# Kernel tuning notes

Measured on AMD Instinct MI355X. Metric: run time of the kernel, lower is better.

The kernel has to match this reference:

```python
import jax, jax.numpy as jnp
import numpy as np

N_NODES = 200000
N_EDGES = 800000
NODE_IN = 133
EDGE_IN = 14
HID = 128
DEPTH = 4
NUM_GRAPHS = 4096


def _linear_init(key, fan_in, fan_out):
    # torch nn.Linear default init: U(-1/sqrt(fan_in), 1/sqrt(fan_in))
    kw, kb = jax.random.split(key)
    bound = 1.0 / np.sqrt(fan_in)
    W = jax.random.uniform(kw, (fan_in, fan_out), jnp.float32, -bound, bound)
    b = jax.random.uniform(kb, (fan_out,), jnp.float32, -bound, bound)
    return W, b


def setup_inputs() -> dict:
    key = jax.random.key(0)
    ks = jax.random.split(key, 8)
    x = jax.random.normal(ks[0], (N_NODES, NODE_IN), jnp.float32)
    edge_index = jax.random.randint(ks[1], (2, N_EDGES), 0, N_NODES, jnp.int64)
    revedge_index = jax.random.randint(ks[2], (N_EDGES,), 0, N_EDGES, jnp.int64)
    edge_attr = jax.random.normal(ks[3], (N_EDGES, EDGE_IN), jnp.float32)
    batch = jnp.sort(jax.random.randint(ks[4], (N_NODES,), 0, NUM_GRAPHS, jnp.int64))
    W1, b1 = _linear_init(ks[5], NODE_IN + EDGE_IN, HID)
    W2, b2 = _linear_init(ks[6], HID, HID)
    W3, b3 = _linear_init(ks[7], NODE_IN + HID, HID)
    return {"x": x, "edge_attr": edge_attr, "W1": W1, "b1": b1, "W2": W2,
            "b2": b2, "W3": W3, "b3": b3, "edge_index": edge_index,
            "revedge_index": revedge_index, "batch": batch,
            "num_graphs": NUM_GRAPHS}


def reference(x, edge_attr, W1, b1, W2, b2, W3, b3,
              edge_index, revedge_index, batch, num_graphs):
    num_nodes = x.shape[0]
    src, dst = edge_index[0], edge_index[1]
    # initial directed edge messages: [E, node_in + edge_in] -> [E, HID]
    init_msg = jnp.concatenate([x[src], edge_attr], axis=1)
    h0 = jax.nn.relu(init_msg @ W1 + b1)
    h = h0
    for _ in range(DEPTH - 1):
        # sum incoming messages at each node, gather back to edges, remove reverse edge
        node_sum = jax.ops.segment_sum(h, dst, num_segments=num_nodes)
        m = node_sum[src] - h[revedge_index]
        h = jax.nn.relu(h0 + m @ W2 + b2)
    # aggregate final edge messages at destination nodes
    v_msg = jax.ops.segment_sum(h, dst, num_segments=num_nodes)
    z = jnp.concatenate([x, v_msg], axis=1)
    node_attr = jax.nn.relu(z @ W3 + b3)  # dropout is identity in eval mode
    # global mean pool over graphs
    sums = jax.ops.segment_sum(node_attr, batch, num_segments=num_graphs)
    counts = jax.ops.segment_sum(jnp.ones((num_nodes,), node_attr.dtype), batch,
                                 num_segments=num_graphs)
    return sums / jnp.maximum(counts, 1.0)[:, None]
```

## Files before the change

kernel.cpp:

```cpp
#include <hip/hip_runtime.h>

#define N_NODES 200000
#define N_EDGES 800000
#define NODE_IN 133
#define EDGE_IN 14
#define HID 128
#define NUM_GRAPHS 4096

#define SCAN_CHUNK 2048
#define SCAN_NBLK ((N_NODES + SCAN_CHUNK - 1) / SCAN_CHUNK)

#define MT 64
#define MT2 128

#define K1_PAD 160
#define K1_STRIDE 168
#define K2_PAD 128
#define K2_STRIDE 136
#define K3_PAD 288
#define K3_STRIDE 296
#define KE_PAD 32
#define KE_STRIDE 40

typedef unsigned short u16;
typedef unsigned char u8;
typedef short bf16x8 __attribute__((ext_vector_type(8)));
typedef float f32x4 __attribute__((ext_vector_type(4)));

__device__ __forceinline__ float bu2f(unsigned s) {
    return __uint_as_float(s << 16);
}
__device__ __forceinline__ u16 f2bu(float f) {
    unsigned u = __float_as_uint(f);
    return (u16)((u + 0x7FFFu + ((u >> 16) & 1u)) >> 16);
}
__device__ __forceinline__ u16 f2bt(float f) {
    return (u16)(__float_as_uint(f) >> 16);
}
__device__ __forceinline__ float e42f(unsigned b) {
    unsigned E = (b >> 4) & 0xF, M = b & 7u;
    if (E == 0) return (float)M * 0.001953125f;
    return __uint_as_float(((E - 7u + 127u) << 23) | (M << 20));
}
__device__ __forceinline__ u8 f2e4(float f) {
    if (!(f > 0.f)) return 0;
    if (f >= 448.f) return 0x7E;
    unsigned u = __float_as_uint(f);
    int e = (int)((u >> 23) & 0xFF) - 127;
    if (e < -6) {
        int q = (int)rintf(f * 512.f);
        return (u8)q;
    }
    unsigned m = u & 0x7FFFFF;
    unsigned keep = m >> 20, rem = m & 0xFFFFF;
    keep += (rem > 0x80000u || (rem == 0x80000u && (keep & 1u))) ? 1u : 0u;
    unsigned E = (unsigned)(e + 7);
    if (keep == 8u) { keep = 0u; E++; }
    return (u8)((E << 4) | keep);
}

#if defined(__has_builtin)
#if __has_builtin(__builtin_amdgcn_cvt_f32_fp8) && __has_builtin(__builtin_amdgcn_cvt_pk_fp8_f32)
#define HW_FP8 1
#endif
#endif

#if defined(HW_FP8)
#define FP8_DEC(dw, s) __builtin_amdgcn_cvt_f32_fp8((int)(dw), (s))
__device__ __forceinline__ unsigned fp8_pk(float a, float b) {
    a = fminf(fmaxf(a, 0.f), 448.f);
    b = fminf(fmaxf(b, 0.f), 448.f);
    return (unsigned)__builtin_amdgcn_cvt_pk_fp8_f32(a, b, 0, false) & 0xFFFFu;
}
#else
#define FP8_DEC(dw, s) e42f(((dw) >> (8 * (s))) & 0xFFu)
__device__ __forceinline__ unsigned fp8_pk(float a, float b) {
    return (unsigned)f2e4(a) | ((unsigned)f2e4(b) << 8);
}
#endif

__device__ __forceinline__ int clampi(int v, int hi) {
    return v < 0 ? 0 : (v >= hi ? hi - 1 : v);
}

__device__ __forceinline__ void acc16(float* a, const uint4 v) {
    a[0]  += FP8_DEC(v.x, 0); a[1]  += FP8_DEC(v.x, 1);
    a[2]  += FP8_DEC(v.x, 2); a[3]  += FP8_DEC(v.x, 3);
    a[4]  += FP8_DEC(v.y, 0); a[5]  += FP8_DEC(v.y, 1);
    a[6]  += FP8_DEC(v.y, 2); a[7]  += FP8_DEC(v.y, 3);
    a[8]  += FP8_DEC(v.z, 0); a[9]  += FP8_DEC(v.z, 1);
    a[10] += FP8_DEC(v.z, 2); a[11] += FP8_DEC(v.z, 3);
    a[12] += FP8_DEC(v.w, 0); a[13] += FP8_DEC(v.w, 1);
    a[14] += FP8_DEC(v.w, 2); a[15] += FP8_DEC(v.w, 3);
}

__global__ __launch_bounds__(256) void k_prep3(const float* __restrict__ W1,
                                               const float* __restrict__ W2,
                                               const float* __restrict__ W3,
                                               u16* __restrict__ WT1,
                                               u16* __restrict__ WT2,
                                               u16* __restrict__ WT3) {
    int idx = blockIdx.x * 256 + threadIdx.x;
    const int n1 = HID * K1_STRIDE, n2 = HID * K2_STRIDE, n3 = HID * K3_STRIDE;
    if (idx < n1) {
        const int n = idx / K1_STRIDE, k = idx % K1_STRIDE;
        WT1[idx] = (k < NODE_IN + EDGE_IN) ? f2bu(W1[k * HID + n]) : (u16)0;
    } else if ((idx -= n1) < n2) {
        const int n = idx / K2_STRIDE, k = idx % K2_STRIDE;
        WT2[idx] = (k < HID) ? f2bu(W2[k * HID + n]) : (u16)0;
    } else if ((idx -= n2) < n3) {
        const int n = idx / K3_STRIDE, k = idx % K3_STRIDE;
        WT3[idx] = (k < NODE_IN + HID) ? f2bu(W3[k * HID + n]) : (u16)0;
    }
}

__global__ __launch_bounds__(256) void k_hist(const int* __restrict__ dst,
                                              int* __restrict__ cnt) {
    const int e = blockIdx.x * 256 + threadIdx.x;
    if (e < N_EDGES) atomicAdd(&cnt[clampi(dst[e], N_NODES)], 1);
}

__global__ __launch_bounds__(256) void k_scan1(const int* __restrict__ cnt,
                                               int* __restrict__ local,
                                               int* __restrict__ partial) {
    __shared__ int tsum[256];
    const int b = blockIdx.x, t = threadIdx.x;
    const int base = b * SCAN_CHUNK + t * 8;
    int v[8];
    int s = 0;
#pragma unroll
    for (int i = 0; i < 8; i++) {
        const int idx = base + i;
        v[i] = (idx < N_NODES) ? cnt[idx] : 0;
        s += v[i];
    }
    tsum[t] = s;
    __syncthreads();
    for (int ofs = 1; ofs < 256; ofs <<= 1) {
        const int add = (t >= ofs) ? tsum[t - ofs] : 0;
        __syncthreads();
        tsum[t] += add;
        __syncthreads();
    }
    int excl = (t == 0) ? 0 : tsum[t - 1];
    if (t == 255) partial[b] = tsum[255];
#pragma unroll
    for (int i = 0; i < 8; i++) {
        const int idx = base + i;
        if (idx < N_NODES) local[idx] = excl;
        excl += v[i];
    }
}

__global__ __launch_bounds__(256) void k_scan2(int* __restrict__ partial) {
    __shared__ int s[256];
    const int t = threadIdx.x;
    s[t] = (t < SCAN_NBLK) ? partial[t] : 0;
    __syncthreads();
    for (int ofs = 1; ofs < 256; ofs <<= 1) {
        const int add = (t >= ofs) ? s[t - ofs] : 0;
        __syncthreads();
        s[t] += add;
        __syncthreads();
    }
    if (t < SCAN_NBLK) partial[t] = (t == 0) ? 0 : s[t - 1];
}

__global__ __launch_bounds__(256) void k_scan3(const int* __restrict__ local,
                                               const int* __restrict__ partial,
                                               int* __restrict__ row_ptr,
                                               int* __restrict__ cursor) {
    const int idx = blockIdx.x * 256 + threadIdx.x;
    if (idx <= N_NODES) {
        const int v = (idx == N_NODES) ? N_EDGES
                                       : local[idx] + partial[idx / SCAN_CHUNK];
        row_ptr[idx] = v;
        if (idx < N_NODES) cursor[idx] = v;
    }
}

__global__ __launch_bounds__(256) void k_place(const int* __restrict__ dst,
                                               int* __restrict__ cursor,
                                               int* __restrict__ eidx,
                                               int* __restrict__ inv) {
    const int e = blockIdx.x * 256 + threadIdx.x;
    if (e < N_EDGES) {
        const int slot = atomicAdd(&cursor[clampi(dst[e], N_NODES)], 1);
        eidx[slot] = e;
        inv[e] = slot;
    }
}

__global__ __launch_bounds__(256) void k_setup(const int* __restrict__ eidx,
                                               const int* __restrict__ src,
                                               const int* __restrict__ rev,
                                               const int* __restrict__ inv,
                                               const float* __restrict__ ea,
                                               int* __restrict__ src_d,
                                               int* __restrict__ rev_d,
                                               u16* __restrict__ ea_d) {
    const int j = blockIdx.x * 256 + threadIdx.x;
    if (j >= N_EDGES) return;
    const int e = clampi(eidx[j], N_EDGES);
    src_d[j] = src[e];
    rev_d[j] = inv[clampi(rev[e], N_EDGES)];
    const float2* er = (const float2*)(ea + (size_t)e * EDGE_IN);
    u16 v[16];
#pragma unroll
    for (int k = 0; k < 7; k++) {
        const float2 u = er[k];
        v[2 * k] = f2bu(u.x);
        v[2 * k + 1] = f2bu(u.y);
    }
    v[14] = 0; v[15] = 0;
    uint4 o1, o2;
    o1.x = (unsigned)v[0] | ((unsigned)v[1] << 16);
    o1.y = (unsigned)v[2] | ((unsigned)v[3] << 16);
    o1.z = (unsigned)v[4] | ((unsigned)v[5] << 16);
    o1.w = (unsigned)v[6] | ((unsigned)v[7] << 16);
    o2.x = (unsigned)v[8] | ((unsigned)v[9] << 16);
    o2.y = (unsigned)v[10] | ((unsigned)v[11] << 16);
    o2.z = (unsigned)v[12] | ((unsigned)v[13] << 16);
    o2.w = 0;
    uint4* dstp = (uint4*)(ea_d + (size_t)j * 16);
    dstp[0] = o1;
    dstp[1] = o2;
}

__global__ __launch_bounds__(256) void k_gather(const u8* __restrict__ h,
                                                const int* __restrict__ row_ptr,
                                                u8* __restrict__ node_sum) {
    const long long idx = (long long)blockIdx.x * 256 + threadIdx.x;
    const int n = (int)(idx >> 3);
    if (n >= N_NODES) return;
    const int c16 = (int)(idx & 7) << 4;
    const int beg = row_ptr[n], end = row_ptr[n + 1];
    float a[16];
#pragma unroll
    for (int i = 0; i < 16; i++) a[i] = 0.f;
    int j = beg;
    for (; j + 4 <= end; j += 4) {
        const uint4 v0 = *(const uint4*)(h + (long long)j * HID + c16);
        const uint4 v1 = *(const uint4*)(h + (long long)(j + 1) * HID + c16);
        const uint4 v2 = *(const uint4*)(h + (long long)(j + 2) * HID + c16);
        const uint4 v3 = *(const uint4*)(h + (long long)(j + 3) * HID + c16);
        acc16(a, v0); acc16(a, v1); acc16(a, v2); acc16(a, v3);
    }
    for (; j < end; j++) {
        const uint4 v = *(const uint4*)(h + (long long)j * HID + c16);
        acc16(a, v);
    }
    uint4 o;
    o.x = fp8_pk(a[0], a[1])   | (fp8_pk(a[2], a[3])   << 16);
    o.y = fp8_pk(a[4], a[5])   | (fp8_pk(a[6], a[7])   << 16);
    o.z = fp8_pk(a[8], a[9])   | (fp8_pk(a[10], a[11]) << 16);
    o.w = fp8_pk(a[12], a[13]) | (fp8_pk(a[14], a[15]) << 16);
    *(uint4*)(node_sum + (long long)n * HID + c16) = o;
}


__global__ __launch_bounds__(256) void k_xw(const float* __restrict__ x,
                                            const u16* __restrict__ WT1,
                                            u16* __restrict__ xw) {
    __shared__ u16 A[MT * K1_STRIDE];
    const int n0 = blockIdx.x * MT;
    const int t = threadIdx.x;
    const int lane = t & 63, wv = t >> 6;
    for (int rr = 0; rr < 16; rr++) {
        const int row = wv * 16 + rr;
        const int n = n0 + row;
        const float* xr = x + (size_t)n * NODE_IN;
        u16* dstr = &A[row * K1_STRIDE];
        dstr[lane] = f2bu(xr[lane]);
        dstr[64 + lane] = f2bu(xr[64 + lane]);
        if (lane < 5) dstr[128 + lane] = f2bu(xr[128 + lane]);
        if (lane < K1_PAD - NODE_IN) dstr[NODE_IN + lane] = 0;
    }
    __syncthreads();

    const int wm = wv & 1, wn = wv >> 1;
    const int lr = lane & 15, lk = (lane >> 4) * 8;
    f32x4 acc[2][4];
#pragma unroll
    for (int m = 0; m < 2; m++)
#pragma unroll
        for (int n = 0; n < 4; n++) acc[m][n] = (f32x4){0.f, 0.f, 0.f, 0.f};

    const int ar0 = (wm * 32 + lr) * K1_STRIDE + lk;
#pragma unroll
    for (int ks = 0; ks < K1_PAD / 32; ks++) {
        const int kk = ks * 32;
        const bf16x8 a0 = *(const bf16x8*)&A[ar0 + kk];
        const bf16x8 a1 = *(const bf16x8*)&A[ar0 + 16 * K1_STRIDE + kk];
#pragma unroll
        for (int n = 0; n < 4; n++) {
            const bf16x8 b = *(const bf16x8*)&WT1[(size_t)(wn * 64 + n * 16 + lr) * K1_STRIDE + kk + lk];
            acc[0][n] = __builtin_amdgcn_mfma_f32_16x16x32_bf16(a0, b, acc[0][n], 0, 0, 0);
            acc[1][n] = __builtin_amdgcn_mfma_f32_16x16x32_bf16(a1, b, acc[1][n], 0, 0, 0);
        }
    }

    const int lr4 = lane >> 4;
#pragma unroll
    for (int n = 0; n < 4; n++) {
        const int col = wn * 64 + n * 16 + lr;
#pragma unroll
        for (int m = 0; m < 2; m++)
#pragma unroll
            for (int j = 0; j < 4; j++) {
                const int nd = n0 + wm * 32 + m * 16 + lr4 * 4 + j;
                xw[(size_t)nd * HID + col] = f2bu(acc[m][n][j]);
            }
    }
}

__global__ __launch_bounds__(256) void k_init3(const u16* __restrict__ xw,
                                               const u16* __restrict__ ea_d,
                                               const u16* __restrict__ WT1,
                                               const float* __restrict__ b1,
                                               const int* __restrict__ src_d,
                                               u8* __restrict__ h0) {
    __shared__ u16 Aea[MT * KE_STRIDE];
    __shared__ u16 W1e[HID * KE_PAD];
    __shared__ u16 Sacc[MT * K2_STRIDE];
    __shared__ float b1s[HID];
    const int e0 = blockIdx.x * MT;
    const int t = threadIdx.x;

    const int prow = t >> 2, pj = t & 3;
    const int ps = clampi(src_d[e0 + prow], N_NODES);
    uint4 xv[4];
#pragma unroll
    for (int q = 0; q < 4; q++)
        xv[q] = *(const uint4*)(xw + (size_t)ps * HID + pj * 32 + q * 8);

    for (int i = t; i < HID * KE_PAD; i += 256) {
        const int n = i >> 5, k = i & 31;
        W1e[i] = (k < EDGE_IN) ? WT1[n * K1_STRIDE + NODE_IN + k] : (u16)0;
    }
    if (t < HID) b1s[t] = b1[t];
    {
        const int row = t >> 2, q = t & 3;
        const uint2 v = *(const uint2*)(ea_d + (size_t)(e0 + row) * 16 + q * 4);
        *(uint2*)&Aea[row * KE_STRIDE + q * 4] = v;
        uint2 z; z.x = 0; z.y = 0;
        *(uint2*)&Aea[row * KE_STRIDE + 16 + q * 4] = z;
    }
    __syncthreads();

    const int lane = t & 63, wid = t >> 6;
    const int wm = wid & 1, wn = wid >> 1;
    const int lr = lane & 15, lk = (lane >> 4) * 8;
    f32x4 acc[2][4];
#pragma unroll
    for (int m = 0; m < 2; m++)
#pragma unroll
        for (int n = 0; n < 4; n++) acc[m][n] = (f32x4){0.f, 0.f, 0.f, 0.f};

    {
        const bf16x8 a0 = *(const bf16x8*)&Aea[(wm * 32 + lr) * KE_STRIDE + lk];
        const bf16x8 a1 = *(const bf16x8*)&Aea[(wm * 32 + 16 + lr) * KE_STRIDE + lk];
#pragma unroll
        for (int n = 0; n < 4; n++) {
            const bf16x8 b = *(const bf16x8*)&W1e[(wn * 64 + n * 16 + lr) * KE_PAD + lk];
            acc[0][n] = __builtin_amdgcn_mfma_f32_16x16x32_bf16(a0, b, acc[0][n], 0, 0, 0);
            acc[1][n] = __builtin_amdgcn_mfma_f32_16x16x32_bf16(a1, b, acc[1][n], 0, 0, 0);
        }
    }

    const int lr4 = lane >> 4;
#pragma unroll
    for (int n = 0; n < 4; n++) {
        const int col = wn * 64 + n * 16 + lr;
#pragma unroll
        for (int m = 0; m < 2; m++)
#pragma unroll
            for (int j = 0; j < 4; j++) {
                const int row = wm * 32 + m * 16 + lr4 * 4 + j;
                Sacc[row * K2_STRIDE + col] = f2bu(acc[m][n][j]);
            }
    }
    __syncthreads();

    const long long e = e0 + prow;
#pragma unroll
    for (int q = 0; q < 4; q++) {
        const int c8 = pj * 32 + q * 8;
        const uint4 sv = *(const uint4*)&Sacc[prow * K2_STRIDE + c8];
        const float4 ba = *(const float4*)&b1s[c8];
        const float4 bbv = *(const float4*)&b1s[c8 + 4];
        const float v0 = bu2f(sv.x & 0xFFFFu) + bu2f(xv[q].x & 0xFFFFu) + ba.x;
        const float v1 = bu2f(sv.x >> 16)     + bu2f(xv[q].x >> 16)     + ba.y;
        const float v2 = bu2f(sv.y & 0xFFFFu) + bu2f(xv[q].y & 0xFFFFu) + ba.z;
        const float v3 = bu2f(sv.y >> 16)     + bu2f(xv[q].y >> 16)     + ba.w;
        const float v4 = bu2f(sv.z & 0xFFFFu) + bu2f(xv[q].z & 0xFFFFu) + bbv.x;
        const float v5 = bu2f(sv.z >> 16)     + bu2f(xv[q].z >> 16)     + bbv.y;
        const float v6 = bu2f(sv.w & 0xFFFFu) + bu2f(xv[q].w & 0xFFFFu) + bbv.z;
        const float v7 = bu2f(sv.w >> 16)     + bu2f(xv[q].w >> 16)     + bbv.w;
        uint2 o;
        o.x = fp8_pk(v0, v1) | (fp8_pk(v2, v3) << 16);
        o.y = fp8_pk(v4, v5) | (fp8_pk(v6, v7) << 16);
        *(uint2*)(h0 + e * HID + c8) = o;
    }
}

__global__ __launch_bounds__(512) void k_msg_mfma(const u8* __restrict__ ns,
                                                  const u8* __restrict__ h,
                                                  const u8* __restrict__ h0g,
                                                  const u16* __restrict__ WT2,
                                                  const float* __restrict__ b2,
                                                  const int* __restrict__ src_d,
                                                  const int* __restrict__ rev_d,
                                                  u8* __restrict__ hn) {
    __shared__ u16 A[MT2 * K2_STRIDE];
    __shared__ float b2s[HID];
    const int e0 = blockIdx.x * MT2;
    const int t = threadIdx.x;

    const int prow = t >> 2, pj = t & 3;
    const long long pe = e0 + prow;
    uint2 h0v[4];
#pragma unroll
    for (int q = 0; q < 4; q++)
        h0v[q] = *(const uint2*)(h0g + pe * HID + pj * 32 + q * 8);

    if (t < HID) b2s[t] = b2[t];
    {
        const int s = clampi(src_d[e0 + prow], N_NODES);
        const int r = clampi(rev_d[e0 + prow], N_EDGES);
        const u8* nsr = ns + (size_t)s * HID + pj * 32;
        const u8* hr = h + (size_t)r * HID + pj * 32;
        u16* dstr = &A[prow * K2_STRIDE + pj * 32];
#pragma unroll
        for (int q = 0; q < 4; q++) {
            const uint2 nv = *(const uint2*)(nsr + q * 8);
            const uint2 hv = *(const uint2*)(hr + q * 8);
            union { bf16x8 v; u16 s[8]; } o;
            o.s[0] = f2bt(FP8_DEC(nv.x, 0) - FP8_DEC(hv.x, 0));
            o.s[1] = f2bt(FP8_DEC(nv.x, 1) - FP8_DEC(hv.x, 1));
            o.s[2] = f2bt(FP8_DEC(nv.x, 2) - FP8_DEC(hv.x, 2));
            o.s[3] = f2bt(FP8_DEC(nv.x, 3) - FP8_DEC(hv.x, 3));
            o.s[4] = f2bt(FP8_DEC(nv.y, 0) - FP8_DEC(hv.y, 0));
            o.s[5] = f2bt(FP8_DEC(nv.y, 1) - FP8_DEC(hv.y, 1));
            o.s[6] = f2bt(FP8_DEC(nv.y, 2) - FP8_DEC(hv.y, 2));
            o.s[7] = f2bt(FP8_DEC(nv.y, 3) - FP8_DEC(hv.y, 3));
            *(bf16x8*)(dstr + q * 8) = o.v;
        }
    }
    __syncthreads();

    const int lane = t & 63, wid = t >> 6;
    const int wm = wid & 3, wn = wid >> 2;
    const int lr = lane & 15, lk = (lane >> 4) * 8;
    f32x4 acc[2][4];
#pragma unroll
    for (int m = 0; m < 2; m++)
#pragma unroll
        for (int n = 0; n < 4; n++) acc[m][n] = (f32x4){0.f, 0.f, 0.f, 0.f};

    const int ar0 = (wm * 32 + lr) * K2_STRIDE + lk;
#pragma unroll
    for (int ks = 0; ks < K2_PAD / 32; ks++) {
        const int kk = ks * 32;
        const bf16x8 a0 = *(const bf16x8*)&A[ar0 + kk];
        const bf16x8 a1 = *(const bf16x8*)&A[ar0 + 16 * K2_STRIDE + kk];
#pragma unroll
        for (int n = 0; n < 4; n++) {
            const bf16x8 b = *(const bf16x8*)&WT2[(size_t)(wn * 64 + n * 16 + lr) * K2_STRIDE + kk + lk];
            acc[0][n] = __builtin_amdgcn_mfma_f32_16x16x32_bf16(a0, b, acc[0][n], 0, 0, 0);
            acc[1][n] = __builtin_amdgcn_mfma_f32_16x16x32_bf16(a1, b, acc[1][n], 0, 0, 0);
        }
    }

    __syncthreads();
    const int lr4 = lane >> 4;
#pragma unroll
    for (int n = 0; n < 4; n++) {
        const int col = wn * 64 + n * 16 + lr;
#pragma unroll
        for (int m = 0; m < 2; m++)
#pragma unroll
            for (int j = 0; j < 4; j++) {
                const int row = wm * 32 + m * 16 + lr4 * 4 + j;
                A[row * K2_STRIDE + col] = f2bt(acc[m][n][j]);
            }
    }
    __syncthreads();

#pragma unroll
    for (int q = 0; q < 4; q++) {
        const int c8 = pj * 32 + q * 8;
        const uint4 sv = *(const uint4*)&A[prow * K2_STRIDE + c8];
        const float4 ba = *(const float4*)&b2s[c8];
        const float4 bbv = *(const float4*)&b2s[c8 + 4];
        const float v0 = bu2f(sv.x & 0xFFFFu) + FP8_DEC(h0v[q].x, 0) + ba.x;
        const float v1 = bu2f(sv.x >> 16)     + FP8_DEC(h0v[q].x, 1) + ba.y;
        const float v2 = bu2f(sv.y & 0xFFFFu) + FP8_DEC(h0v[q].x, 2) + ba.z;
        const float v3 = bu2f(sv.y >> 16)     + FP8_DEC(h0v[q].x, 3) + ba.w;
        const float v4 = bu2f(sv.z & 0xFFFFu) + FP8_DEC(h0v[q].y, 0) + bbv.x;
        const float v5 = bu2f(sv.z >> 16)     + FP8_DEC(h0v[q].y, 1) + bbv.y;
        const float v6 = bu2f(sv.w & 0xFFFFu) + FP8_DEC(h0v[q].y, 2) + bbv.z;
        const float v7 = bu2f(sv.w >> 16)     + FP8_DEC(h0v[q].y, 3) + bbv.w;
        uint2 o;
        o.x = fp8_pk(v0, v1) | (fp8_pk(v2, v3) << 16);
        o.y = fp8_pk(v4, v5) | (fp8_pk(v6, v7) << 16);
        *(uint2*)(hn + pe * HID + c8) = o;
    }
}

__global__ __launch_bounds__(512) void k_node_mfma(const float* __restrict__ x,
                                                   const u8* __restrict__ h,
                                                   const int* __restrict__ row_ptr,
                                                   const u16* __restrict__ WT3,
                                                   const float* __restrict__ b3,
                                                   u16* __restrict__ node_attr) {
    __shared__ u16 A[MT * K3_STRIDE];
    const int n0 = blockIdx.x * MT;
    const int t = threadIdx.x;
    const int lane = t & 63, wv = t >> 6;
    const int wm = wv & 1, wn = wv >> 1;
    const int lr = lane & 15, lk = (lane >> 4) * 8;

    {
        const int vrow = wv * 8 + (lane >> 3);
        const int vn = n0 + vrow;
        const int c16 = (lane & 7) << 4;
        const int beg = row_ptr[vn], end = row_ptr[vn + 1];
        float a[16];
#pragma unroll
        for (int i = 0; i < 16; i++) a[i] = 0.f;
        int j = beg;
        for (; j + 4 <= end; j += 4) {
            const uint4 v0 = *(const uint4*)(h + (long long)j * HID + c16);
            const uint4 v1 = *(const uint4*)(h + (long long)(j + 1) * HID + c16);
            const uint4 v2 = *(const uint4*)(h + (long long)(j + 2) * HID + c16);
            const uint4 v3 = *(const uint4*)(h + (long long)(j + 3) * HID + c16);
            acc16(a, v0); acc16(a, v1); acc16(a, v2); acc16(a, v3);
        }
        for (; j < end; j++) {
            const uint4 v = *(const uint4*)(h + (long long)j * HID + c16);
            acc16(a, v);
        }
        u16* vd = &A[vrow * K3_STRIDE + NODE_IN + c16];
#pragma unroll
        for (int i = 0; i < 16; i++) vd[i] = f2bt(a[i]);
    }

    for (int rr = 0; rr < 8; rr++) {
        const int row = wv * 8 + rr;
        const int n = n0 + row;
        const float* xr = x + (size_t)n * NODE_IN;
        u16* dstr = &A[row * K3_STRIDE];
        dstr[lane] = f2bu(xr[lane]);
        dstr[64 + lane] = f2bu(xr[64 + lane]);
        if (lane < 5) dstr[128 + lane] = f2bu(xr[128 + lane]);
        if (lane < K3_PAD - (NODE_IN + HID))
            dstr[NODE_IN + HID + lane] = 0;
    }
    __syncthreads();

    f32x4 acc[2][2];
#pragma unroll
    for (int m = 0; m < 2; m++)
#pragma unroll
        for (int n = 0; n < 2; n++) acc[m][n] = (f32x4){0.f, 0.f, 0.f, 0.f};
    const int ar0 = (wm * 32 + lr) * K3_STRIDE + lk;

    for (int ks = 0; ks < K3_PAD / 32; ks++) {
        const int kk = ks * 32;
        const bf16x8 a0 = *(const bf16x8*)&A[ar0 + kk];
        const bf16x8 a1 = *(const bf16x8*)&A[ar0 + 16 * K3_STRIDE + kk];
#pragma unroll
        for (int n = 0; n < 2; n++) {
            const bf16x8 b = *(const bf16x8*)&WT3[(size_t)(wn * 32 + n * 16 + lr) * K3_STRIDE + kk + lk];
            acc[0][n] = __builtin_amdgcn_mfma_f32_16x16x32_bf16(a0, b, acc[0][n], 0, 0, 0);
            acc[1][n] = __builtin_amdgcn_mfma_f32_16x16x32_bf16(a1, b, acc[1][n], 0, 0, 0);
        }
    }

    const int lr4 = lane >> 4;
#pragma unroll
    for (int n = 0; n < 2; n++) {
        const int col = wn * 32 + n * 16 + lr;
        const float bias = b3[col];
#pragma unroll
        for (int m = 0; m < 2; m++)
#pragma unroll
            for (int j = 0; j < 4; j++) {
                const int nd = n0 + wm * 32 + m * 16 + lr4 * 4 + j;
                float v = acc[m][n][j] + bias;
                node_attr[(size_t)nd * HID + col] = f2bu(v > 0.f ? v : 0.f);
            }
    }
}

__global__ __launch_bounds__(128) void k_pool2(const u16* __restrict__ node_attr,
                                               const int* __restrict__ batch,
                                               float* __restrict__ out) {
    const int g = blockIdx.x;
    __shared__ int lo_s, hi_s;
    if (threadIdx.x == 0) {
        int lo = 0, hi = N_NODES;
        while (lo < hi) { int mid = (lo + hi) >> 1; if (batch[mid] < g) lo = mid + 1; else hi = mid; }
        lo_s = lo;
        int lo2 = lo, hi2 = N_NODES;
        while (lo2 < hi2) { int mid = (lo2 + hi2) >> 1; if (batch[mid] <= g) lo2 = mid + 1; else hi2 = mid; }
        hi_s = lo2;
    }
    __syncthreads();
    const int lo = lo_s, hi = hi_s;
    float acc = 0.f;
    for (int n = lo; n < hi; n++)
        acc += bu2f(node_attr[(size_t)n * HID + threadIdx.x]);
    const float cnt = (hi > lo) ? (float)(hi - lo) : 1.f;
    out[(size_t)g * HID + threadIdx.x] = acc / cnt;
}

extern "C" void kernel_launch(void* const* d_in, const int* in_sizes, int n_in,
                              void* d_out, int out_size, void* d_ws, size_t ws_size,
                              hipStream_t stream) {
    const float* x   = (const float*)d_in[0];
    const float* ea  = (const float*)d_in[1];
    const float* W1  = (const float*)d_in[2];
    const float* b1  = (const float*)d_in[3];
    const float* W2  = (const float*)d_in[4];
    const float* b2  = (const float*)d_in[5];
    const float* W3  = (const float*)d_in[6];
    const float* b3  = (const float*)d_in[7];
    const int*   ei  = (const int*)d_in[8];
    const int*   src = ei;
    const int*   dst = ei + N_EDGES;
    const int*   rev = (const int*)d_in[9];
    const int*   bat = (const int*)d_in[10];

    char* ws = (char*)d_ws;
    size_t off = 0;
    auto alloc = [&](size_t bytes) -> void* {
        void* p = ws + off;
        off += (bytes + 255) & ~(size_t)255;
        return p;
    };
    const size_t hbytes = (size_t)N_EDGES * HID;
    u8* h0 = (u8*)alloc(hbytes);
    u8* hA = (u8*)alloc(hbytes);
    u8* hB = (u8*)alloc(hbytes);
    u8* node_sum = (u8*)alloc((size_t)N_NODES * HID);
    int* row_ptr = (int*)alloc((size_t)(N_NODES + 1) * sizeof(int));
    int* eidx = (int*)alloc((size_t)N_EDGES * sizeof(int));
    int* src_d = (int*)alloc((size_t)N_EDGES * sizeof(int));
    int* rev_d = (int*)alloc((size_t)N_EDGES * sizeof(int));
    u16* ea_d = (u16*)alloc((size_t)N_EDGES * 16 * sizeof(u16));
    u16* WT1 = (u16*)alloc((size_t)HID * K1_STRIDE * sizeof(u16));
    u16* WT2 = (u16*)alloc((size_t)HID * K2_STRIDE * sizeof(u16));
    u16* WT3 = (u16*)alloc((size_t)HID * K3_STRIDE * sizeof(u16));
    u16* xw = (u16*)hA;
    u16* node_attr = (u16*)h0;

    if (ws_size < off) return;

    k_prep3<<<(HID * (K1_STRIDE + K2_STRIDE + K3_STRIDE) + 255) / 256, 256, 0,
              stream>>>(W1, W2, W3, WT1, WT2, WT3);

    {
        int* cnt = (int*)node_sum;
        int* local = cnt + N_NODES;
        int* cursor = local + N_NODES;
        int* partial = cursor + N_NODES;
        int* inv = partial + 4096;
        hipMemsetAsync(cnt, 0, (size_t)N_NODES * sizeof(int), stream);
        k_hist<<<(N_EDGES + 255) / 256, 256, 0, stream>>>(dst, cnt);
        k_scan1<<<SCAN_NBLK, 256, 0, stream>>>(cnt, local, partial);
        k_scan2<<<1, 256, 0, stream>>>(partial);
        k_scan3<<<(N_NODES + 256) / 256, 256, 0, stream>>>(local, partial, row_ptr, cursor);
        k_place<<<(N_EDGES + 255) / 256, 256, 0, stream>>>(dst, cursor, eidx, inv);
        k_setup<<<(N_EDGES + 255) / 256, 256, 0, stream>>>(eidx, src, rev, inv, ea, src_d, rev_d, ea_d);
    }

    k_xw<<<N_NODES / MT, 256, 0, stream>>>(x, WT1, xw);
    k_init3<<<N_EDGES / MT, 256, 0, stream>>>(xw, ea_d, WT1, b1, src_d, h0);

    const u8* h = h0;
    u8* bufs[2] = {hA, hB};
    const int agg_blocks = (int)(((long long)N_NODES * 8 + 255) / 256);
    for (int it = 0; it < 3; it++) {
        k_gather<<<agg_blocks, 256, 0, stream>>>(h, row_ptr, node_sum);
        u8* hn = bufs[it & 1];
        k_msg_mfma<<<N_EDGES / MT2, 512, 0, stream>>>(node_sum, h, h0, WT2, b2, src_d, rev_d, hn);
        h = hn;
    }

    k_node_mfma<<<N_NODES / MT, 512, 0, stream>>>(x, h, row_ptr, WT3, b3, node_attr);
    k_pool2<<<NUM_GRAPHS, 128, 0, stream>>>(node_attr, bat, (float*)d_out);
}
```

Baseline: 815.7 us.

## Fuse node-sum aggregation into message kernel with boundary fix-up pass

The message kernel now keeps its freshly computed edge messages in shared memory and reduces them per destination node for nodes whose incoming edges fall entirely inside the block's 128-edge tile. The result is written to a second node-sum buffer. A lightweight fix-up kernel then handles only the nodes whose edge range crosses a tile boundary, or that have no incoming edges. This replaces the full gather kernel for iterations two and three, avoiding a re-read of the whole edge-message array. The cost is extra shared memory, a dst array built in setup, and the fix-up kernel, which still reads every row_ptr entry.

```diff
diff --git a/kernel.cpp b/kernel.cpp
--- a/kernel.cpp
+++ b/kernel.cpp
@@ -92,6 +92,14 @@
     a[10] += FP8_DEC(v.z, 2); a[11] += FP8_DEC(v.z, 3);
     a[12] += FP8_DEC(v.w, 0); a[13] += FP8_DEC(v.w, 1);
     a[14] += FP8_DEC(v.w, 2); a[15] += FP8_DEC(v.w, 3);
+}
+__device__ __forceinline__ uint4 pk16(const float* a) {
+    uint4 o;
+    o.x = fp8_pk(a[0], a[1])   | (fp8_pk(a[2], a[3])   << 16);
+    o.y = fp8_pk(a[4], a[5])   | (fp8_pk(a[6], a[7])   << 16);
+    o.z = fp8_pk(a[8], a[9])   | (fp8_pk(a[10], a[11]) << 16);
+    o.w = fp8_pk(a[12], a[13]) | (fp8_pk(a[14], a[15]) << 16);
+    return o;
 }
 
 __global__ __launch_bounds__(256) void k_prep3(const float* __restrict__ W1,
@@ -193,17 +201,20 @@
 
 __global__ __launch_bounds__(256) void k_setup(const int* __restrict__ eidx,
                                                const int* __restrict__ src,
+                                               const int* __restrict__ dst,
                                                const int* __restrict__ rev,
                                                const int* __restrict__ inv,
                                                const float* __restrict__ ea,
                                                int* __restrict__ src_d,
                                                int* __restrict__ rev_d,
+                                               int* __restrict__ dst_d,
                                                u16* __restrict__ ea_d) {
     const int j = blockIdx.x * 256 + threadIdx.x;
     if (j >= N_EDGES) return;
     const int e = clampi(eidx[j], N_EDGES);
     src_d[j] = src[e];
     rev_d[j] = inv[clampi(rev[e], N_EDGES)];
+    dst_d[j] = clampi(dst[e], N_NODES);
     const float2* er = (const float2*)(ea + (size_t)e * EDGE_IN);
     u16 v[16];
 #pragma unroll
@@ -250,12 +261,26 @@
         const uint4 v = *(const uint4*)(h + (long long)j * HID + c16);
         acc16(a, v);
     }
-    uint4 o;
-    o.x = fp8_pk(a[0], a[1])   | (fp8_pk(a[2], a[3])   << 16);
-    o.y = fp8_pk(a[4], a[5])   | (fp8_pk(a[6], a[7])   << 16);
-    o.z = fp8_pk(a[8], a[9])   | (fp8_pk(a[10], a[11]) << 16);
-    o.w = fp8_pk(a[12], a[13]) | (fp8_pk(a[14], a[15]) << 16);
-    *(uint4*)(node_sum + (long long)n * HID + c16) = o;
+    *(uint4*)(node_sum + (long long)n * HID + c16) = pk16(a);
+}
+
+__global__ __launch_bounds__(256) void k_fix(const u8* __restrict__ hn,
+                                             const int* __restrict__ row_ptr,
+                                             u8* __restrict__ ns_out) {
+    const long long idx = (long long)blockIdx.x * 256 + threadIdx.x;
+    const int n = (int)(idx >> 3);
+    if (n >= N_NODES) return;
+    const int c16 = (int)(idx & 7) << 4;
+    const int beg = row_ptr[n], end = row_ptr[n + 1];
+    if (beg < end && (beg >> 7) == ((end - 1) >> 7)) return;
+    float a[16];
+#pragma unroll
+    for (int i = 0; i < 16; i++) a[i] = 0.f;
+    for (int j = beg; j < end; j++) {
+        const uint4 v = *(const uint4*)(hn + (long long)j * HID + c16);
+        acc16(a, v);
+    }
+    *(uint4*)(ns_out + (long long)n * HID + c16) = pk16(a);
 }
 
 
@@ -404,6 +429,7 @@
     }
 }
 
+template <bool FUSE_NS>
 __global__ __launch_bounds__(512) void k_msg_mfma(const u8* __restrict__ ns,
                                                   const u8* __restrict__ h,
                                                   const u8* __restrict__ h0g,
@@ -411,8 +437,12 @@
                                                   const float* __restrict__ b2,
                                                   const int* __restrict__ src_d,
                                                   const int* __restrict__ rev_d,
-                                                  u8* __restrict__ hn) {
+                                                  const int* __restrict__ row_ptr,
+                                                  const int* __restrict__ dst_d,
+                                                  u8* __restrict__ hn,
+                                                  u8* __restrict__ ns_out) {
     __shared__ u16 A[MT2 * K2_STRIDE];
+    __shared__ __align__(16) u8 HN[FUSE_NS ? MT2 * HID : 16];
     __shared__ float b2s[HID];
     const int e0 = blockIdx.x * MT2;
     const int t = threadIdx.x;
@@ -505,6 +535,28 @@
         o.x = fp8_pk(v0, v1) | (fp8_pk(v2, v3) << 16);
         o.y = fp8_pk(v4, v5) | (fp8_pk(v6, v7) << 16);
         *(uint2*)(hn + pe * HID + c8) = o;
+        if (FUSE_NS) *(uint2*)(HN + prow * HID + c8) = o;
+    }
+
+    if (FUSE_NS) {
+        __syncthreads();
+        const int nfirst = dst_d[e0];
+        const int nlast = dst_d[e0 + MT2 - 1];
+        const int slot = t >> 3;
+        const int c16 = (t & 7) << 4;
+        for (int n = nfirst + slot; n <= nlast; n += 64) {
+            const int beg = row_ptr[n], end = row_ptr[n + 1];
+            if (beg < end && beg >= e0 && end <= e0 + MT2) {
+                float a[16];
+#pragma unroll
+                for (int i = 0; i < 16; i++) a[i] = 0.f;
+                for (int j = beg; j < end; j++) {
+                    const uint4 v = *(const uint4*)(HN + (j - e0) * HID + c16);
+                    acc16(a, v);
+                }
+                *(uint4*)(ns_out + (long long)n * HID + c16) = pk16(a);
+            }
+        }
     }
 }
 
@@ -644,11 +696,13 @@
     u8* h0 = (u8*)alloc(hbytes);
     u8* hA = (u8*)alloc(hbytes);
     u8* hB = (u8*)alloc(hbytes);
-    u8* node_sum = (u8*)alloc((size_t)N_NODES * HID);
+    u8* nsA = (u8*)alloc((size_t)N_NODES * HID);
+    u8* nsB = (u8*)alloc((size_t)N_NODES * HID);
     int* row_ptr = (int*)alloc((size_t)(N_NODES + 1) * sizeof(int));
     int* eidx = (int*)alloc((size_t)N_EDGES * sizeof(int));
     int* src_d = (int*)alloc((size_t)N_EDGES * sizeof(int));
     int* rev_d = (int*)alloc((size_t)N_EDGES * sizeof(int));
+    int* dst_d = (int*)alloc((size_t)N_EDGES * sizeof(int));
     u16* ea_d = (u16*)alloc((size_t)N_EDGES * 16 * sizeof(u16));
     u16* WT1 = (u16*)alloc((size_t)HID * K1_STRIDE * sizeof(u16));
     u16* WT2 = (u16*)alloc((size_t)HID * K2_STRIDE * sizeof(u16));
@@ -662,7 +716,7 @@
               stream>>>(W1, W2, W3, WT1, WT2, WT3);
 
     {
-        int* cnt = (int*)node_sum;
+        int* cnt = (int*)nsA;
         int* local = cnt + N_NODES;
         int* cursor = local + N_NODES;
         int* partial = cursor + N_NODES;
@@ -673,22 +727,26 @@
         k_scan2<<<1, 256, 0, stream>>>(partial);
         k_scan3<<<(N_NODES + 256) / 256, 256, 0, stream>>>(local, partial, row_ptr, cursor);
         k_place<<<(N_EDGES + 255) / 256, 256, 0, stream>>>(dst, cursor, eidx, inv);
-        k_setup<<<(N_EDGES + 255) / 256, 256, 0, stream>>>(eidx, src, rev, inv, ea, src_d, rev_d, ea_d);
+        k_setup<<<(N_EDGES + 255) / 256, 256, 0, stream>>>(eidx, src, dst, rev, inv, ea,
+                                                           src_d, rev_d, dst_d, ea_d);
     }
 
     k_xw<<<N_NODES / MT, 256, 0, stream>>>(x, WT1, xw);
     k_init3<<<N_EDGES / MT, 256, 0, stream>>>(xw, ea_d, WT1, b1, src_d, h0);
 
-    const u8* h = h0;
-    u8* bufs[2] = {hA, hB};
     const int agg_blocks = (int)(((long long)N_NODES * 8 + 255) / 256);
-    for (int it = 0; it < 3; it++) {
-        k_gather<<<agg_blocks, 256, 0, stream>>>(h, row_ptr, node_sum);
-        u8* hn = bufs[it & 1];
-        k_msg_mfma<<<N_EDGES / MT2, 512, 0, stream>>>(node_sum, h, h0, WT2, b2, src_d, rev_d, hn);
-        h = hn;
-    }
-
-    k_node_mfma<<<N_NODES / MT, 512, 0, stream>>>(x, h, row_ptr, WT3, b3, node_attr);
+    const int msg_blocks = N_EDGES / MT2;
+
+    k_gather<<<agg_blocks, 256, 0, stream>>>(h0, row_ptr, nsA);
+    k_msg_mfma<true><<<msg_blocks, 512, 0, stream>>>(nsA, h0, h0, WT2, b2, src_d,
+                                                     rev_d, row_ptr, dst_d, hA, nsB);
+    k_fix<<<agg_blocks, 256, 0, stream>>>(hA, row_ptr, nsB);
+    k_msg_mfma<true><<<msg_blocks, 512, 0, stream>>>(nsB, hA, h0, WT2, b2, src_d,
+                                                     rev_d, row_ptr, dst_d, hB, nsA);
+    k_fix<<<agg_blocks, 256, 0, stream>>>(hB, row_ptr, nsA);
+    k_msg_mfma<false><<<msg_blocks, 512, 0, stream>>>(nsA, hB, h0, WT2, b2, src_d,
+                                                      rev_d, row_ptr, dst_d, hA, nsB);
+
+    k_node_mfma<<<N_NODES / MT, 512, 0, stream>>>(x, hA, row_ptr, WT3, b3, node_attr);
     k_pool2<<<NUM_GRAPHS, 128, 0, stream>>>(node_attr, bat, (float*)d_out);
 }
```

Result: slower. 874.1 us (+7.2%).
